# Performance work log

Measured on AMD Instinct MI355X. Metric: run time of the kernel, lower is better.

Reference implementation:

```python
import jax, jax.numpy as jnp
import numpy as np

B, N, F, H = 64, 1024, 128, 256  # graphs, nodes per graph, nfeat, nhid


def setup_inputs() -> dict:
    key = jax.random.key(0)
    ks = jax.random.split(key, 8)
    s_in = 1.0 / np.sqrt(F)
    s_h = 1.0 / np.sqrt(H)
    return {
        "embs": jax.random.normal(ks[0], (B, N, F), jnp.float32),
        "adjmat": jax.random.uniform(ks[1], (B, N, N), jnp.float32) / N,  # row-scaled dense adjacency
        "W0": jax.random.normal(ks[2], (F, H), jnp.float32) * s_in,
        "b0": jnp.zeros((H,), jnp.float32),
        "W1": jax.random.normal(ks[3], (H, H), jnp.float32) * s_h,
        "b1": jnp.zeros((H,), jnp.float32),
        "W2": jax.random.normal(ks[4], (H, H), jnp.float32) * s_h,
        "b2": jnp.zeros((H,), jnp.float32),
        "Wl": jax.random.normal(ks[5], (H, F), jnp.float32) * s_h,
        "bl": jnp.zeros((F,), jnp.float32),
    }


def reference(embs, adjmat, W0, b0, W1, b1, W2, b2, Wl, bl):
    # Batched form of the per-graph loop: every adj is N x N, so the
    # x[:adj.shape[0]] slice is identity and all graphs fuse into one GEMM.
    hid = embs  # [B, N, F]
    for W, b in ((W0, b0), (W1, b1), (W2, b2)):
        # GraphConvolution: adj @ (x @ W) + b, then relu
        hid = jax.nn.relu(jnp.einsum('bnm,bmh->bnh', adjmat, hid @ W) + b)
    out = hid @ Wl + bl          # [B, N, F] linear_hid
    return out[:, 0, :]          # hid[0] per graph -> [B, F]
```

## Files before the change

kernel.cpp:

```cpp
#include <hip/hip_runtime.h>
#include <stdint.h>

typedef __bf16 bf16;
typedef __bf16 bf16x8 __attribute__((ext_vector_type(8)));
typedef float f32x4 __attribute__((ext_vector_type(4)));

enum { EPI_STORE = 0, EPI_BIAS_RELU = 1, EPI_VRED = 2 };

__device__ __forceinline__ void gload16(const bf16* g, bf16* l) {
  __builtin_amdgcn_global_load_lds(
      (const __attribute__((address_space(1))) unsigned int*)g,
      (__attribute__((address_space(3))) unsigned int*)l, 16, 0, 0);
}

template<int EPI>
__global__ __launch_bounds__(256, 2)
void gemm_bt(const bf16* __restrict__ Ap, const bf16* __restrict__ Btp,
             const float* __restrict__ bias, bf16* __restrict__ C,
             float* __restrict__ vpart, const float* __restrict__ adjp,
             int K, int ldA, int ldBt, int ldC,
             long sA, long sBt, long sC)
{
  constexpr int BM = 128, BN = 256, BK = 32;
  static_assert(BM / 64 + BN / 64 == 6, "vmcnt(6) assumes 6 gloads/thread/step");
  __shared__ __align__(16) bf16 As[2][BM * BK];
  __shared__ __align__(16) bf16 Bs[2][BN * BK];
  __shared__ float a0s[BM];
  __shared__ float vsum[BN];

  const int tid  = threadIdx.x;
  const int lane = tid & 63;
  const int wid  = tid >> 6;
  const int wm   = wid >> 1;
  const int wn   = wid & 1;
  const int l15  = lane & 15;
  const int quad = lane >> 4;

  const int nb = blockIdx.x, mb = blockIdx.y, g = blockIdx.z;

  const long aoff = (long)g * sA + (long)mb * BM * ldA;
  const long boff = (long)g * sBt + (long)nb * BN * ldBt;

  if constexpr (EPI == EPI_VRED) {
    if (tid < BM) a0s[tid] = adjp[(long)g * sA + mb * BM + tid];
    vsum[tid] = 0.f;
  }

  const int r   = tid >> 2;
  const int kcs = (((tid & 3) ^ ((tid >> 3) & 3)) << 3);

  const bf16* Ag0 = Ap + aoff;
  const bf16* Bg0 = Btp + boff;

  auto issueG = [&](int s, int buf) {
    const int k0 = s * BK;
    #pragma unroll
    for (int p = 0; p < BM / 64; ++p)
      gload16(Ag0 + (long)(p * 64 + r) * ldA + k0 + kcs, &As[buf][p * 2048 + tid * 8]);
    #pragma unroll
    for (int p = 0; p < BN / 64; ++p)
      gload16(Bg0 + (long)(p * 64 + r) * ldBt + k0 + kcs, &Bs[buf][p * 2048 + tid * 8]);
  };

  const int csw = ((quad ^ ((l15 >> 1) & 3)) << 3);

  f32x4 acc[4][8] = {};
  const int nsteps = K / BK;

  issueG(0, 0);
  int cur = 0;
  for (int s = 0; s < nsteps; ++s) {
    if (s + 1 < nsteps) {
      issueG(s + 1, cur ^ 1);
      asm volatile("s_waitcnt vmcnt(6)" ::: "memory");
    } else {
      asm volatile("s_waitcnt vmcnt(0)" ::: "memory");
    }
    __builtin_amdgcn_s_barrier();

    bf16x8 af[4], bfr[8];
    #pragma unroll
    for (int i = 0; i < 4; ++i)
      af[i] = *(const bf16x8*)&As[cur][(wm * 64 + i * 16 + l15) * BK + csw];
    #pragma unroll
    for (int j = 0; j < 8; ++j)
      bfr[j] = *(const bf16x8*)&Bs[cur][(wn * 128 + j * 16 + l15) * BK + csw];
    asm volatile("s_waitcnt lgkmcnt(0)" ::: "memory");
    __builtin_amdgcn_s_barrier();

    #pragma unroll
    for (int i = 0; i < 4; ++i)
      #pragma unroll
      for (int j = 0; j < 8; ++j)
        acc[i][j] = __builtin_amdgcn_mfma_f32_16x16x32_bf16(af[i], bfr[j], acc[i][j], 0, 0, 0);
    cur ^= 1;
  }

  if constexpr (EPI == EPI_STORE || EPI == EPI_BIAS_RELU) {
    bf16* Cg = C + (long)g * sC;
    #pragma unroll
    for (int i = 0; i < 4; ++i) {
      const int row0 = mb * BM + wm * 64 + i * 16 + quad * 4;
      #pragma unroll
      for (int j = 0; j < 8; ++j) {
        const int col = nb * BN + wn * 128 + j * 16 + l15;
        float bv = 0.f;
        if constexpr (EPI == EPI_BIAS_RELU) bv = bias[col];
        #pragma unroll
        for (int rr = 0; rr < 4; ++rr) {
          float v = acc[i][j][rr];
          if constexpr (EPI == EPI_BIAS_RELU) v = fmaxf(v + bv, 0.f);
          Cg[(long)(row0 + rr) * ldC + col] = (bf16)v;
        }
      }
    }
  } else {
    __syncthreads();
    #pragma unroll
    for (int j = 0; j < 8; ++j) {
      const int col = wn * 128 + j * 16 + l15;
      const float bv = bias[col];
      float p = 0.f;
      #pragma unroll
      for (int i = 0; i < 4; ++i) {
        const int lr = wm * 64 + i * 16 + quad * 4;
        #pragma unroll
        for (int rr = 0; rr < 4; ++rr)
          p += fmaxf(acc[i][j][rr] + bv, 0.f) * a0s[lr + rr];
      }
      atomicAdd(&vsum[col], p);
    }
    __syncthreads();
    vpart[((long)g * 8 + mb) * 256 + tid] = vsum[tid];
  }
}

__global__ void cvt2(const float* __restrict__ a, bf16* __restrict__ ao, long na8,
                     const float* __restrict__ b, bf16* __restrict__ bo, long nb8)
{
  const long stride = (long)gridDim.x * blockDim.x;
  for (long i = (long)blockIdx.x * blockDim.x + threadIdx.x; i < na8 + nb8; i += stride) {
    const float* src; bf16* dst; long k;
    if (i < na8) { src = a; dst = ao; k = i; } else { src = b; dst = bo; k = i - na8; }
    const float4* s = (const float4*)(src + k * 8);
    float4 v0 = s[0], v1 = s[1];
    bf16x8 w;
    w[0]=(bf16)v0.x; w[1]=(bf16)v0.y; w[2]=(bf16)v0.z; w[3]=(bf16)v0.w;
    w[4]=(bf16)v1.x; w[5]=(bf16)v1.y; w[6]=(bf16)v1.z; w[7]=(bf16)v1.w;
    *(bf16x8*)(dst + k * 8) = w;
  }
}

__global__ void prep_w(const float* __restrict__ W0, const float* __restrict__ W1,
                       bf16* __restrict__ W0t, bf16* __restrict__ W1t)
{
  const int idx = blockIdx.x * 256 + threadIdx.x;
  if (idx < 256 * 128) {
    const int h = idx >> 7, k = idx & 127;
    W0t[idx] = (bf16)W0[k * 256 + h];
  }
  const int h = idx >> 8, k = idx & 255;
  W1t[idx] = (bf16)W1[k * 256 + h];
}

__global__ void finish_k(const float* __restrict__ vpart, const float* __restrict__ W2,
                         const float* __restrict__ b2, const float* __restrict__ Wl,
                         const float* __restrict__ bl, float* __restrict__ out)
{
  const int b = blockIdx.x, t = threadIdx.x;
  __shared__ float v[256], h3[256];
  float s = 0.f;
  #pragma unroll
  for (int mb = 0; mb < 8; ++mb) s += vpart[((long)b * 8 + mb) * 256 + t];
  v[t] = s;
  __syncthreads();
  float z = b2[t];
  for (int k = 0; k < 256; ++k) z += v[k] * W2[k * 256 + t];
  h3[t] = fmaxf(z, 0.f);
  __syncthreads();
  if (t < 128) {
    float o = bl[t];
    for (int h = 0; h < 256; ++h) o += h3[h] * Wl[h * 128 + t];
    out[(long)b * 128 + t] = o;
  }
}

extern "C" void kernel_launch(void* const* d_in, const int* in_sizes, int n_in,
                              void* d_out, int out_size, void* d_ws, size_t ws_size,
                              hipStream_t stream) {
  const float* embs = (const float*)d_in[0];
  const float* adj  = (const float*)d_in[1];
  const float* W0   = (const float*)d_in[2];
  const float* b0   = (const float*)d_in[3];
  const float* W1   = (const float*)d_in[4];
  const float* b1   = (const float*)d_in[5];
  const float* W2   = (const float*)d_in[6];
  const float* b2   = (const float*)d_in[7];
  const float* Wl   = (const float*)d_in[8];
  const float* bl   = (const float*)d_in[9];
  float* out = (float*)d_out;

  char* ws = (char*)d_ws;
  bf16*  Zt     = (bf16*)(ws);
  bf16*  Hb     = (bf16*)(ws + 33554432);
  bf16*  W0t    = (bf16*)(ws + 67108864);
  bf16*  W1t    = (bf16*)(ws + 67174400);
  float* vpart  = (float*)(ws + 67305472);
  bf16*  embs16 = (bf16*)(ws + 67829760);
  bf16*  adj16  = (bf16*)(ws + 134217728);

  prep_w<<<256, 256, 0, stream>>>(W0, W1, W0t, W1t);

  cvt2<<<2048, 256, 0, stream>>>(adj, adj16, 64L * 1024 * 1024 / 8,
                                 embs, embs16, 64L * 1024 * 128 / 8);

  gemm_bt<EPI_STORE><<<dim3(4, 2, 64), 256, 0, stream>>>(
      W0t, embs16, nullptr, Zt, nullptr, nullptr,
      128, 128, 128, 1024, 0L, 131072L, 262144L);

  gemm_bt<EPI_BIAS_RELU><<<dim3(1, 8, 64), 256, 0, stream>>>(
      adj16, Zt, b0, Hb, nullptr, nullptr,
      1024, 1024, 1024, 256, 1048576L, 262144L, 262144L);

  gemm_bt<EPI_STORE><<<dim3(4, 2, 64), 256, 0, stream>>>(
      W1t, Hb, nullptr, Zt, nullptr, nullptr,
      256, 256, 256, 1024, 0L, 262144L, 262144L);

  gemm_bt<EPI_VRED><<<dim3(1, 8, 64), 256, 0, stream>>>(
      adj16, Zt, b1, nullptr, vpart, adj,
      1024, 1024, 1024, 256, 1048576L, 262144L, 0L);

  finish_k<<<64, 256, 0, stream>>>(vpart, W2, b2, Wl, bl, out);
}
```

Measured before the change: 616.3 us.

## Fuse fp32 adjacency conversion into first aggregation GEMM and triple-buffer loads

Drops the separate fp32→bf16 conversion pass over the adjacency matrix. The first adjacency GEMM now loads fp32 tiles into registers, converts them, writes them to LDS, and also writes the bf16 copy to global memory for reuse by the second adjacency GEMM. The GEMM pipeline moves from double to triple buffering, with deeper vmcnt waits so two steps are in flight. This saves one full read of the 256MB fp32 adjacency, at the cost of more LDS, more register pressure and scattered global stores inside the GEMM loop.

```diff
diff --git a/kernel.cpp b/kernel.cpp
--- a/kernel.cpp
+++ b/kernel.cpp
@@ -13,18 +13,18 @@
       (__attribute__((address_space(3))) unsigned int*)l, 16, 0, 0);
 }
 
-template<int EPI>
+template<bool A_F32, int EPI, bool WRITE_A16>
 __global__ __launch_bounds__(256, 2)
-void gemm_bt(const bf16* __restrict__ Ap, const bf16* __restrict__ Btp,
+void gemm_bt(const void* __restrict__ Ap, const bf16* __restrict__ Btp,
              const float* __restrict__ bias, bf16* __restrict__ C,
              float* __restrict__ vpart, const float* __restrict__ adjp,
+             bf16* __restrict__ A16,
              int K, int ldA, int ldBt, int ldC,
              long sA, long sBt, long sC)
 {
   constexpr int BM = 128, BN = 256, BK = 32;
-  static_assert(BM / 64 + BN / 64 == 6, "vmcnt(6) assumes 6 gloads/thread/step");
-  __shared__ __align__(16) bf16 As[2][BM * BK];
-  __shared__ __align__(16) bf16 Bs[2][BN * BK];
+  __shared__ __align__(16) bf16 As[3][BM * BK];
+  __shared__ __align__(16) bf16 Bs[3][BN * BK];
   __shared__ float a0s[BM];
   __shared__ float vsum[BN];
 
@@ -47,53 +47,112 @@
   }
 
   const int r   = tid >> 2;
-  const int kcs = (((tid & 3) ^ ((tid >> 3) & 3)) << 3);
-
-  const bf16* Ag0 = Ap + aoff;
+  const int c4  = tid & 3;
+  const int sw  = (r >> 1) & 3;
+  const int kcs = (c4 ^ sw) << 3;
+  const int kcp = c4 << 3;
+  const int csw = (quad ^ ((l15 >> 1) & 3)) << 3;
+
   const bf16* Bg0 = Btp + boff;
 
-  auto issueG = [&](int s, int buf) {
-    const int k0 = s * BK;
-    #pragma unroll
-    for (int p = 0; p < BM / 64; ++p)
-      gload16(Ag0 + (long)(p * 64 + r) * ldA + k0 + kcs, &As[buf][p * 2048 + tid * 8]);
-    #pragma unroll
-    for (int p = 0; p < BN / 64; ++p)
-      gload16(Bg0 + (long)(p * 64 + r) * ldBt + k0 + kcs, &Bs[buf][p * 2048 + tid * 8]);
-  };
-
-  const int csw = ((quad ^ ((l15 >> 1) & 3)) << 3);
+  auto issueB = [&](int s, int buf) {
+    const bf16* Bg = Bg0 + s * BK;
+    #pragma unroll
+    for (int p = 0; p < 4; ++p)
+      gload16(Bg + (long)(p * 64 + r) * ldBt + kcs, &Bs[buf][p * 2048 + tid * 8]);
+  };
+  auto issueAg = [&](int s, int buf) {
+    const bf16* Ag = (const bf16*)Ap + aoff + s * BK;
+    #pragma unroll
+    for (int p = 0; p < 2; ++p)
+      gload16(Ag + (long)(p * 64 + r) * ldA + kcs, &As[buf][p * 2048 + tid * 8]);
+  };
+  auto issueAf = [&](int s, float4 (&pf)[4]) {
+    const float* Ag = (const float*)Ap + aoff + s * BK;
+    #pragma unroll
+    for (int p = 0; p < 2; ++p) {
+      const float4* src = (const float4*)(Ag + (long)(p * 64 + r) * ldA + kcp);
+      pf[p * 2 + 0] = src[0];
+      pf[p * 2 + 1] = src[1];
+    }
+  };
+  auto commitAf = [&](int s, float4 (&pf)[4], int buf) {
+    #pragma unroll
+    for (int p = 0; p < 2; ++p) {
+      float4 v0 = pf[p * 2 + 0], v1 = pf[p * 2 + 1];
+      bf16x8 w;
+      w[0]=(bf16)v0.x; w[1]=(bf16)v0.y; w[2]=(bf16)v0.z; w[3]=(bf16)v0.w;
+      w[4]=(bf16)v1.x; w[5]=(bf16)v1.y; w[6]=(bf16)v1.z; w[7]=(bf16)v1.w;
+      *(bf16x8*)&As[buf][p * 2048 + r * 32 + kcs] = w;
+      if constexpr (WRITE_A16)
+        *(bf16x8*)&A16[aoff + (long)(p * 64 + r) * ldA + s * BK + kcp] = w;
+    }
+  };
 
   f32x4 acc[4][8] = {};
-  const int nsteps = K / BK;
-
-  issueG(0, 0);
-  int cur = 0;
-  for (int s = 0; s < nsteps; ++s) {
-    if (s + 1 < nsteps) {
-      issueG(s + 1, cur ^ 1);
-      asm volatile("s_waitcnt vmcnt(6)" ::: "memory");
-    } else {
-      asm volatile("s_waitcnt vmcnt(0)" ::: "memory");
-    }
-    __builtin_amdgcn_s_barrier();
-
-    bf16x8 af[4], bfr[8];
-    #pragma unroll
-    for (int i = 0; i < 4; ++i)
-      af[i] = *(const bf16x8*)&As[cur][(wm * 64 + i * 16 + l15) * BK + csw];
-    #pragma unroll
-    for (int j = 0; j < 8; ++j)
-      bfr[j] = *(const bf16x8*)&Bs[cur][(wn * 128 + j * 16 + l15) * BK + csw];
+  const int n = K / BK;
+
+  if constexpr (!A_F32) {
+    issueAg(0, 0); issueB(0, 0);
+    if (n > 1) { issueAg(1, 1); issueB(1, 1); }
+    for (int s = 0; s < n; ++s) {
+      const int b = s % 3;
+      if (s + 2 < n) { issueAg(s + 2, (s + 2) % 3); issueB(s + 2, (s + 2) % 3); }
+      if (s + 2 < n)      asm volatile("s_waitcnt vmcnt(12)" ::: "memory");
+      else if (s + 1 < n) asm volatile("s_waitcnt vmcnt(6)"  ::: "memory");
+      else                asm volatile("s_waitcnt vmcnt(0)"  ::: "memory");
+      __builtin_amdgcn_s_barrier();
+
+      bf16x8 af[4], bfr[8];
+      #pragma unroll
+      for (int i = 0; i < 4; ++i)
+        af[i] = *(const bf16x8*)&As[b][(wm * 64 + i * 16 + l15) * 32 + csw];
+      #pragma unroll
+      for (int j = 0; j < 8; ++j)
+        bfr[j] = *(const bf16x8*)&Bs[b][(wn * 128 + j * 16 + l15) * 32 + csw];
+      asm volatile("s_waitcnt lgkmcnt(0)" ::: "memory");
+      __builtin_amdgcn_s_barrier();
+
+      #pragma unroll
+      for (int i = 0; i < 4; ++i)
+        #pragma unroll
+        for (int j = 0; j < 8; ++j)
+          acc[i][j] = __builtin_amdgcn_mfma_f32_16x16x32_bf16(af[i], bfr[j], acc[i][j], 0, 0, 0);
+    }
+  } else {
+    float4 pfa[4], pfb[4];
+    issueAf(0, pfa); issueB(0, 0);
+    issueAf(1, pfb); issueB(1, 1);
+    commitAf(0, pfa, 0);
     asm volatile("s_waitcnt lgkmcnt(0)" ::: "memory");
     __builtin_amdgcn_s_barrier();
 
-    #pragma unroll
-    for (int i = 0; i < 4; ++i)
+    auto bodyF = [&](int s, float4 (&pfI)[4], float4 (&pfC)[4]) {
+      const int b = s % 3;
+      if (s + 2 < n) { issueAf(s + 2, pfI); issueB(s + 2, (s + 2) % 3); }
+      if (s + 2 < n)      asm volatile("s_waitcnt vmcnt(16)" ::: "memory");
+      else if (s + 1 < n) asm volatile("s_waitcnt vmcnt(8)"  ::: "memory");
+      else                asm volatile("s_waitcnt vmcnt(0)"  ::: "memory");
+      __builtin_amdgcn_s_barrier();
+
+      bf16x8 af[4], bfr[8];
+      #pragma unroll
+      for (int i = 0; i < 4; ++i)
+        af[i] = *(const bf16x8*)&As[b][(wm * 64 + i * 16 + l15) * 32 + csw];
       #pragma unroll
       for (int j = 0; j < 8; ++j)
-        acc[i][j] = __builtin_amdgcn_mfma_f32_16x16x32_bf16(af[i], bfr[j], acc[i][j], 0, 0, 0);
-    cur ^= 1;
+        bfr[j] = *(const bf16x8*)&Bs[b][(wn * 128 + j * 16 + l15) * 32 + csw];
+      if (s + 1 < n) commitAf(s + 1, pfC, (s + 1) % 3);
+      asm volatile("s_waitcnt lgkmcnt(0)" ::: "memory");
+      __builtin_amdgcn_s_barrier();
+
+      #pragma unroll
+      for (int i = 0; i < 4; ++i)
+        #pragma unroll
+        for (int j = 0; j < 8; ++j)
+          acc[i][j] = __builtin_amdgcn_mfma_f32_16x16x32_bf16(af[i], bfr[j], acc[i][j], 0, 0, 0);
+    };
+    for (int s = 0; s < n; s += 2) { bodyF(s, pfa, pfb); bodyF(s + 1, pfb, pfa); }
   }
 
   if constexpr (EPI == EPI_STORE || EPI == EPI_BIAS_RELU) {
@@ -135,19 +194,16 @@
   }
 }
 
-__global__ void cvt2(const float* __restrict__ a, bf16* __restrict__ ao, long na8,
-                     const float* __restrict__ b, bf16* __restrict__ bo, long nb8)
+__global__ void cvt1(const float* __restrict__ src, bf16* __restrict__ dst, long n8)
 {
   const long stride = (long)gridDim.x * blockDim.x;
-  for (long i = (long)blockIdx.x * blockDim.x + threadIdx.x; i < na8 + nb8; i += stride) {
-    const float* src; bf16* dst; long k;
-    if (i < na8) { src = a; dst = ao; k = i; } else { src = b; dst = bo; k = i - na8; }
-    const float4* s = (const float4*)(src + k * 8);
+  for (long i = (long)blockIdx.x * blockDim.x + threadIdx.x; i < n8; i += stride) {
+    const float4* s = (const float4*)(src + i * 8);
     float4 v0 = s[0], v1 = s[1];
     bf16x8 w;
     w[0]=(bf16)v0.x; w[1]=(bf16)v0.y; w[2]=(bf16)v0.z; w[3]=(bf16)v0.w;
     w[4]=(bf16)v1.x; w[5]=(bf16)v1.y; w[6]=(bf16)v1.z; w[7]=(bf16)v1.w;
-    *(bf16x8*)(dst + k * 8) = w;
+    *(bf16x8*)(dst + i * 8) = w;
   }
 }
 
@@ -210,24 +266,22 @@
   bf16*  adj16  = (bf16*)(ws + 134217728);
 
   prep_w<<<256, 256, 0, stream>>>(W0, W1, W0t, W1t);
-
-  cvt2<<<2048, 256, 0, stream>>>(adj, adj16, 64L * 1024 * 1024 / 8,
-                                 embs, embs16, 64L * 1024 * 128 / 8);
-
-  gemm_bt<EPI_STORE><<<dim3(4, 2, 64), 256, 0, stream>>>(
-      W0t, embs16, nullptr, Zt, nullptr, nullptr,
+  cvt1<<<2048, 256, 0, stream>>>(embs, embs16, 64L * 1024 * 128 / 8);
+
+  gemm_bt<false, EPI_STORE, false><<<dim3(4, 2, 64), 256, 0, stream>>>(
+      W0t, embs16, nullptr, Zt, nullptr, nullptr, nullptr,
       128, 128, 128, 1024, 0L, 131072L, 262144L);
 
-  gemm_bt<EPI_BIAS_RELU><<<dim3(1, 8, 64), 256, 0, stream>>>(
-      adj16, Zt, b0, Hb, nullptr, nullptr,
+  gemm_bt<true, EPI_BIAS_RELU, true><<<dim3(1, 8, 64), 256, 0, stream>>>(
+      adj, Zt, b0, Hb, nullptr, nullptr, adj16,
       1024, 1024, 1024, 256, 1048576L, 262144L, 262144L);
 
-  gemm_bt<EPI_STORE><<<dim3(4, 2, 64), 256, 0, stream>>>(
-      W1t, Hb, nullptr, Zt, nullptr, nullptr,
+  gemm_bt<false, EPI_STORE, false><<<dim3(4, 2, 64), 256, 0, stream>>>(
+      W1t, Hb, nullptr, Zt, nullptr, nullptr, nullptr,
       256, 256, 256, 1024, 0L, 262144L, 262144L);
 
-  gemm_bt<EPI_VRED><<<dim3(1, 8, 64), 256, 0, stream>>>(
-      adj16, Zt, b1, nullptr, vpart, adj,
+  gemm_bt<false, EPI_VRED, false><<<dim3(1, 8, 64), 256, 0, stream>>>(
+      adj16, Zt, b1, nullptr, vpart, adj, nullptr,
       1024, 1024, 1024, 256, 1048576L, 262144L, 0L);
 
   finish_k<<<64, 256, 0, stream>>>(vpart, W2, b2, Wl, bl, out);
```

Measured after the change: 601.7 us. 2.4% less time.
